# Kernel optimization log

Measured on AMD Instinct MI355X. Metric: run time of the kernel, lower is better.

## Reference

```python
import jax, jax.numpy as jnp
import numpy as np

EMBEDDING_DIM = 10
CONTEXT_SIZE_1 = 1
CONTEXT_SIZE_2 = 3
VOCAB = 50000
N = 1_000_000
NUM_NUMERIC = 16


def setup_inputs() -> dict:
    key = jax.random.key(0)
    ks = jax.random.split(key, 9)
    text_1 = jax.random.randint(ks[0], (N,), 0, VOCAB)
    text_2 = jax.random.randint(ks[1], (N,), 0, VOCAB)
    numeric_features = jax.random.normal(ks[2], (N, NUM_NUMERIC), dtype=jnp.float32)
    emb_table_1 = jax.random.normal(ks[3], (VOCAB, EMBEDDING_DIM), dtype=jnp.float32)
    emb_table_2 = jax.random.normal(ks[4], (VOCAB, EMBEDDING_DIM), dtype=jnp.float32)
    d_in = 2 * EMBEDDING_DIM + NUM_NUMERIC
    W1 = jax.random.normal(ks[5], (d_in, 128), dtype=jnp.float32) / np.sqrt(d_in)
    b1 = jnp.zeros((128,), dtype=jnp.float32)
    W2 = jax.random.normal(ks[6], (128, 1), dtype=jnp.float32) / np.sqrt(128.0)
    b2 = jnp.zeros((1,), dtype=jnp.float32)
    return {
        "text_1": text_1,
        "text_2": text_2,
        "numeric_features": numeric_features,
        "emb_table_1": emb_table_1,
        "emb_table_2": emb_table_2,
        "W1": W1,
        "b1": b1,
        "W2": W2,
        "b2": b2,
    }


def _contextual_embedding(ids, table, context_size):
    # mean of embeddings over window [i-cs, i+cs], clipped at sequence edges
    n = ids.shape[0]
    emb = table[ids]  # [N, D] gather
    # prefix sums with leading zero row: S[j] = sum(emb[0:j])
    S = jnp.concatenate([jnp.zeros((1, emb.shape[1]), emb.dtype),
                         jnp.cumsum(emb, axis=0)], axis=0)
    pos = jnp.arange(n)
    lo = jnp.maximum(pos - context_size, 0)
    hi = jnp.minimum(pos + context_size + 1, n)
    wsum = S[hi] - S[lo]                       # [N, D]
    count = (hi - lo).astype(emb.dtype)[:, None]
    return wsum / count


def reference(text_1, text_2, numeric_features, emb_table_1, emb_table_2, W1, b1, W2, b2):
    embed_1 = _contextual_embedding(text_1, emb_table_1, CONTEXT_SIZE_1)  # [N, 10]
    embed_2 = _contextual_embedding(text_2, emb_table_2, CONTEXT_SIZE_2)  # [N, 10]
    combined = jnp.concatenate([embed_1, embed_2, numeric_features], axis=1)
    h = jax.nn.relu(combined @ W1 + b1)
    out = h @ W2 + b2
    return jax.nn.sigmoid(out)  # [N, 1]
```

## Files before the change

### kernel.cpp

```cpp
#include <hip/hip_runtime.h>
#include <hip/hip_bf16.h>

#define EMB 10
#define DIN 36
#define HID 128
#define BM  128

typedef __attribute__((ext_vector_type(8))) short short8;
typedef __attribute__((ext_vector_type(4))) float f32x4;

__device__ __forceinline__ short bf16_hi(float v) {
  __hip_bfloat16 h = __float2bfloat16(v);
  return *reinterpret_cast<short*>(&h);
}
__device__ __forceinline__ float bf16_to_f(short s) {
  __hip_bfloat16 h = *reinterpret_cast<__hip_bfloat16*>(&s);
  return __bfloat162float(h);
}

__global__ void prep_kernel(const float* __restrict__ W1, const float* __restrict__ b1,
                            short* __restrict__ Bpack) {
  int b = blockIdx.x;
  int term = b >> 4;
  int ct   = (b >> 1) & 7;
  int ks   = b & 1;
  int l = threadIdx.x;
  int col = ct * 16 + (l & 15);
  int kb  = ks * 32 + (l >> 4) * 8;
  short8 o;
#pragma unroll
  for (int e = 0; e < 8; ++e) {
    int k = kb + e;
    float v = 0.0f;
    if (k < DIN)       v = W1[k * HID + col];
    else if (k == DIN) v = b1[col];
    short hb = bf16_hi(v);
    o[e] = (term == 0) ? hb : bf16_hi(v - bf16_to_f(hb));
  }
  *(short8*)(Bpack + (size_t)(((term * 8 + ct) * 2 + ks) * 64 + l) * 8) = o;
}

__global__ __launch_bounds__(256)
void fused_kernel(const int* __restrict__ t1, const int* __restrict__ t2,
                  const float* __restrict__ numf,
                  const float* __restrict__ tab1, const float* __restrict__ tab2,
                  const short* __restrict__ Bpack,
                  const float* __restrict__ W2, const float* __restrict__ b2,
                  float* __restrict__ out, int N) {
  __shared__ float E1[BM + 2][11];
  __shared__ float E2[BM + 6][11];
  __shared__ float Cs[BM][38];
  __shared__ float W2s[HID];

  const int tid = threadIdx.x;
  const long base = (long)blockIdx.x * BM;
  const int rloc = tid & 127;
  const int half = tid >> 7;
  const long rowm = base + rloc;

  float4 nfa, nfb;
  if (rowm < (long)N) {
    const float4* np = (const float4*)(numf + rowm * 16 + half * 8);
    nfa = np[0]; nfb = np[1];
  }

  if (tid < BM + 2) {
    long g = base - 1 + tid;
    if (g >= 0 && g < (long)N) {
      const float2* src = (const float2*)(tab1 + (long)t1[g] * EMB);
#pragma unroll
      for (int i = 0; i < 5; ++i) {
        float2 v = src[i];
        E1[tid][2 * i] = v.x; E1[tid][2 * i + 1] = v.y;
      }
    } else {
#pragma unroll
      for (int i = 0; i < EMB; ++i) E1[tid][i] = 0.0f;
    }
  }
  {
    int h = tid - (256 - (BM + 6));
    if (h >= 0) {
      long g = base - 3 + h;
      if (g >= 0 && g < (long)N) {
        const float2* src = (const float2*)(tab2 + (long)t2[g] * EMB);
#pragma unroll
        for (int i = 0; i < 5; ++i) {
          float2 v = src[i];
          E2[h][2 * i] = v.x; E2[h][2 * i + 1] = v.y;
        }
      } else {
#pragma unroll
        for (int i = 0; i < EMB; ++i) E2[h][i] = 0.0f;
      }
    }
  }
  if (tid < HID) W2s[tid] = W2[tid];
  __syncthreads();

  if (tid < 120) {
    int grp = tid / 10, d = tid - grp * 10;
    int r0 = grp * 11;
    float e[13];
#pragma unroll
    for (int i = 0; i < 13; ++i) {
      int h = r0 + i; if (h > 129) h = 129;
      e[i] = E1[h][d];
    }
#pragma unroll
    for (int i = 0; i < 11; ++i) {
      int rr = r0 + i;
      if (rr < BM) {
        long row = base + rr;
        float inv = 1.0f / 3.0f;
        if (row == 0 || row >= (long)N - 1) {
          long lo = row - 1; if (lo < 0) lo = 0;
          long hi = row + 2; if (hi > (long)N) hi = (long)N;
          long c = hi - lo;  if (c < 1) c = 1;
          inv = 1.0f / (float)c;
        }
        Cs[rr][d] = (e[i] + e[i + 1] + e[i + 2]) * inv;
      }
    }
  } else if (tid < 250) {
    int u = tid - 120;
    int grp = u / 10, d = u - grp * 10;
    int r0 = grp * 10;
    float e[16];
#pragma unroll
    for (int i = 0; i < 16; ++i) {
      int h = r0 + i; if (h > 133) h = 133;
      e[i] = E2[h][d];
    }
    float w = e[0] + e[1] + e[2] + e[3] + e[4] + e[5] + e[6];
#pragma unroll
    for (int i = 0; i < 10; ++i) {
      int rr = r0 + i;
      if (rr < BM) {
        long row = base + rr;
        float inv = 1.0f / 7.0f;
        if (row < 3 || row >= (long)N - 3) {
          long lo = row - 3; if (lo < 0) lo = 0;
          long hi = row + 4; if (hi > (long)N) hi = (long)N;
          long c = hi - lo;  if (c < 1) c = 1;
          inv = 1.0f / (float)c;
        }
        Cs[rr][10 + d] = w * inv;
      }
      if (i < 9) w += e[i + 7] - e[i];
    }
  }
  if (rowm < (long)N) {
    float* cp = &Cs[rloc][20 + half * 8];
    *(float2*)(cp + 0) = make_float2(nfa.x, nfa.y);
    *(float2*)(cp + 2) = make_float2(nfa.z, nfa.w);
    *(float2*)(cp + 4) = make_float2(nfb.x, nfb.y);
    *(float2*)(cp + 6) = make_float2(nfb.z, nfb.w);
    if (half == 0) *(float2*)(&Cs[rloc][36]) = make_float2(1.0f, 0.0f);
  }
  __syncthreads();

  const int wid = tid >> 6;
  const int l = tid & 63;
  const int arow = l & 15;
  const int kg = l >> 4;

  short8 aHi[2][2], aLo[2][2];
#pragma unroll
  for (int rtl = 0; rtl < 2; ++rtl) {
    const int r = (wid * 2 + rtl) * 16 + arow;
    const float* crow = &Cs[r][0];
    {
      float v[8];
#pragma unroll
      for (int i = 0; i < 4; ++i) {
        float2 t = *(const float2*)(crow + kg * 8 + 2 * i);
        v[2 * i] = t.x; v[2 * i + 1] = t.y;
      }
#pragma unroll
      for (int e = 0; e < 8; ++e) {
        short hb = bf16_hi(v[e]);
        aHi[rtl][0][e] = hb;
        aLo[rtl][0][e] = bf16_hi(v[e] - bf16_to_f(hb));
      }
    }
    if (kg == 0) {
      float v[8];
#pragma unroll
      for (int i = 0; i < 3; ++i) {
        float2 t = *(const float2*)(crow + 32 + 2 * i);
        v[2 * i] = t.x; v[2 * i + 1] = t.y;
      }
      v[6] = 0.0f; v[7] = 0.0f;
#pragma unroll
      for (int e = 0; e < 8; ++e) {
        short hb = bf16_hi(v[e]);
        aHi[rtl][1][e] = hb;
        aLo[rtl][1][e] = bf16_hi(v[e] - bf16_to_f(hb));
      }
    } else {
#pragma unroll
      for (int e = 0; e < 8; ++e) { aHi[rtl][1][e] = 0; aLo[rtl][1][e] = 0; }
    }
  }

  float part[2][4] = {{0,0,0,0},{0,0,0,0}};
#pragma unroll
  for (int ct = 0; ct < 8; ++ct) {
    short8 bb[2][2];
#pragma unroll
    for (int term = 0; term < 2; ++term)
#pragma unroll
      for (int ks = 0; ks < 2; ++ks)
        bb[term][ks] = *(const short8*)(Bpack +
            (size_t)(((term * 8 + ct) * 2 + ks) * 64 + l) * 8);
    float w2c = W2s[ct * 16 + (l & 15)];
#pragma unroll
    for (int rtl = 0; rtl < 2; ++rtl) {
      f32x4 acc = {0.0f, 0.0f, 0.0f, 0.0f};
#pragma unroll
      for (int ks = 0; ks < 2; ++ks) {
        acc = __builtin_amdgcn_mfma_f32_16x16x32_bf16(aHi[rtl][ks], bb[0][ks], acc, 0, 0, 0);
        acc = __builtin_amdgcn_mfma_f32_16x16x32_bf16(aLo[rtl][ks], bb[0][ks], acc, 0, 0, 0);
        acc = __builtin_amdgcn_mfma_f32_16x16x32_bf16(aHi[rtl][ks], bb[1][ks], acc, 0, 0, 0);
      }
#pragma unroll
      for (int r = 0; r < 4; ++r) {
        float hv = fmaxf(acc[r], 0.0f);
        part[rtl][r] += hv * w2c;
      }
    }
  }
#pragma unroll
  for (int off = 1; off < 16; off <<= 1) {
#pragma unroll
    for (int rtl = 0; rtl < 2; ++rtl)
#pragma unroll
      for (int r = 0; r < 4; ++r)
        part[rtl][r] += __shfl_xor(part[rtl][r], off, 64);
  }
  if ((l & 15) < 4) {
    float b2v = b2[0];
#pragma unroll
    for (int rtl = 0; rtl < 2; ++rtl) {
      int rt = wid * 2 + rtl;
      long grow = base + rt * 16 + (l >> 4) * 4 + (l & 15);
      if (grow < (long)N) {
        float x = part[rtl][l & 15] + b2v;
        out[grow] = 1.0f / (1.0f + expf(-x));
      }
    }
  }
}

extern "C" void kernel_launch(void* const* d_in, const int* in_sizes, int n_in,
                              void* d_out, int out_size, void* d_ws, size_t ws_size,
                              hipStream_t stream) {
  const int*   t1   = (const int*)d_in[0];
  const int*   t2   = (const int*)d_in[1];
  const float* numf = (const float*)d_in[2];
  const float* tab1 = (const float*)d_in[3];
  const float* tab2 = (const float*)d_in[4];
  const float* W1   = (const float*)d_in[5];
  const float* b1   = (const float*)d_in[6];
  const float* W2   = (const float*)d_in[7];
  const float* b2   = (const float*)d_in[8];
  float* out = (float*)d_out;
  const int N = in_sizes[0];
  short* Bpack = (short*)d_ws;

  hipLaunchKernelGGL(prep_kernel, dim3(32), dim3(64), 0, stream, W1, b1, Bpack);
  int nblk = (N + BM - 1) / BM;
  hipLaunchKernelGGL(fused_kernel, dim3(nblk), dim3(256), 0, stream,
                     t1, t2, numf, tab1, tab2, Bpack, W2, b2, out, N);
}
```

Before: 182.1 us.

## Load numeric features straight into MFMA registers, bypass LDS staging

Each lane now reads the numeric-feature columns it needs for its MFMA A fragments directly from global memory into registers, instead of staging them through the shared Cs tile, which shrinks from 38 to 22 columns. The hi/lo bf16 split is replaced with a truncation-based split using byte permutes. The window-sum edge handling moves to a block-level branch so interior blocks skip per-row boundary checks. The sigmoid uses exp2f. The trade-offs are less coalesced per-lane global loads and a truncating rather than rounding hi part, which the lo term should compensate for.

```diff
diff --git a/kernel.cpp b/kernel.cpp
--- a/kernel.cpp
+++ b/kernel.cpp
@@ -9,6 +9,8 @@
 typedef __attribute__((ext_vector_type(8))) short short8;
 typedef __attribute__((ext_vector_type(4))) float f32x4;
 
+union U8 { unsigned u[4]; short8 v; };
+
 __device__ __forceinline__ short bf16_hi(float v) {
   __hip_bfloat16 h = __float2bfloat16(v);
   return *reinterpret_cast<short*>(&h);
@@ -16,6 +18,14 @@
 __device__ __forceinline__ float bf16_to_f(short s) {
   __hip_bfloat16 h = *reinterpret_cast<__hip_bfloat16*>(&s);
   return __bfloat162float(h);
+}
+
+__device__ __forceinline__ void split_pair(float a, float b, unsigned &hi, unsigned &lo) {
+  unsigned ua = __float_as_uint(a), ub = __float_as_uint(b);
+  hi = __builtin_amdgcn_perm(ub, ua, 0x07060302u);
+  float ra = a - __uint_as_float(ua & 0xFFFF0000u);
+  float rb = b - __uint_as_float(ub & 0xFFFF0000u);
+  lo = __builtin_amdgcn_perm(__float_as_uint(rb), __float_as_uint(ra), 0x07060302u);
 }
 
 __global__ void prep_kernel(const float* __restrict__ W1, const float* __restrict__ b1,
@@ -47,24 +57,35 @@
                   const short* __restrict__ Bpack,
                   const float* __restrict__ W2, const float* __restrict__ b2,
                   float* __restrict__ out, int N) {
-  __shared__ float E1[BM + 2][11];
-  __shared__ float E2[BM + 6][11];
-  __shared__ float Cs[BM][38];
+  __shared__ float E1[134][11];
+  __shared__ float E2[136][11];
+  __shared__ float Cs[BM][22];
   __shared__ float W2s[HID];
 
   const int tid = threadIdx.x;
   const long base = (long)blockIdx.x * BM;
-  const int rloc = tid & 127;
-  const int half = tid >> 7;
-  const long rowm = base + rloc;
-
-  float4 nfa, nfb;
-  if (rowm < (long)N) {
-    const float4* np = (const float4*)(numf + rowm * 16 + half * 8);
-    nfa = np[0]; nfb = np[1];
-  }
-
-  if (tid < BM + 2) {
+  const int wid = tid >> 6;
+  const int l = tid & 63;
+  const int arow = l & 15;
+  const int kg = l >> 4;
+
+  const long rg0 = base + (long)(wid * 2) * 16 + arow;
+  const long rg1 = rg0 + 16;
+  float4 qa0 = {0,0,0,0}, qa1 = {0,0,0,0}, qb0 = {0,0,0,0}, qb1 = {0,0,0,0};
+  if (kg == 0) {
+    if (rg0 < (long)N) qa0 = *(const float4*)(numf + rg0 * 16 + 12);
+    if (rg1 < (long)N) qa1 = *(const float4*)(numf + rg1 * 16 + 12);
+  } else if (kg == 2) {
+    if (rg0 < (long)N) qa0 = *(const float4*)(numf + rg0 * 16);
+    if (rg1 < (long)N) qa1 = *(const float4*)(numf + rg1 * 16);
+  } else if (kg == 3) {
+    if (rg0 < (long)N) { qa0 = *(const float4*)(numf + rg0 * 16 + 4);
+                         qb0 = *(const float4*)(numf + rg0 * 16 + 8); }
+    if (rg1 < (long)N) { qa1 = *(const float4*)(numf + rg1 * 16 + 4);
+                         qb1 = *(const float4*)(numf + rg1 * 16 + 8); }
+  }
+
+  if (tid < 130) {
     long g = base - 1 + tid;
     if (g >= 0 && g < (long)N) {
       const float2* src = (const float2*)(tab1 + (long)t1[g] * EMB);
@@ -79,7 +100,7 @@
     }
   }
   {
-    int h = tid - (256 - (BM + 6));
+    int h = tid - 122;
     if (h >= 0) {
       long g = base - 3 + h;
       if (g >= 0 && g < (long)N) {
@@ -95,31 +116,33 @@
       }
     }
   }
-  if (tid < HID) W2s[tid] = W2[tid];
+  if (tid >= 128) W2s[tid - 128] = W2[tid - 128];
   __syncthreads();
 
+  const bool edgeblk = (base == 0) || (base + BM + 3 > (long)N);
   if (tid < 120) {
     int grp = tid / 10, d = tid - grp * 10;
     int r0 = grp * 11;
     float e[13];
 #pragma unroll
-    for (int i = 0; i < 13; ++i) {
-      int h = r0 + i; if (h > 129) h = 129;
-      e[i] = E1[h][d];
-    }
-#pragma unroll
-    for (int i = 0; i < 11; ++i) {
-      int rr = r0 + i;
-      if (rr < BM) {
-        long row = base + rr;
-        float inv = 1.0f / 3.0f;
-        if (row == 0 || row >= (long)N - 1) {
+    for (int i = 0; i < 13; ++i) e[i] = E1[r0 + i][d];
+    if (!edgeblk) {
+#pragma unroll
+      for (int i = 0; i < 11; ++i) {
+        int rr = r0 + i;
+        if (rr < BM) Cs[rr][d] = (e[i] + e[i + 1] + e[i + 2]) * (1.0f / 3.0f);
+      }
+    } else {
+#pragma unroll
+      for (int i = 0; i < 11; ++i) {
+        int rr = r0 + i;
+        if (rr < BM) {
+          long row = base + rr;
           long lo = row - 1; if (lo < 0) lo = 0;
           long hi = row + 2; if (hi > (long)N) hi = (long)N;
           long c = hi - lo;  if (c < 1) c = 1;
-          inv = 1.0f / (float)c;
+          Cs[rr][d] = (e[i] + e[i + 1] + e[i + 2]) / (float)c;
         }
-        Cs[rr][d] = (e[i] + e[i + 1] + e[i + 2]) * inv;
       }
     }
   } else if (tid < 250) {
@@ -128,80 +151,70 @@
     int r0 = grp * 10;
     float e[16];
 #pragma unroll
-    for (int i = 0; i < 16; ++i) {
-      int h = r0 + i; if (h > 133) h = 133;
-      e[i] = E2[h][d];
-    }
+    for (int i = 0; i < 16; ++i) e[i] = E2[r0 + i][d];
     float w = e[0] + e[1] + e[2] + e[3] + e[4] + e[5] + e[6];
-#pragma unroll
-    for (int i = 0; i < 10; ++i) {
-      int rr = r0 + i;
-      if (rr < BM) {
-        long row = base + rr;
-        float inv = 1.0f / 7.0f;
-        if (row < 3 || row >= (long)N - 3) {
+    if (!edgeblk) {
+#pragma unroll
+      for (int i = 0; i < 10; ++i) {
+        int rr = r0 + i;
+        if (rr < BM) Cs[rr][10 + d] = w * (1.0f / 7.0f);
+        if (i < 9) w += e[i + 7] - e[i];
+      }
+    } else {
+#pragma unroll
+      for (int i = 0; i < 10; ++i) {
+        int rr = r0 + i;
+        if (rr < BM) {
+          long row = base + rr;
           long lo = row - 3; if (lo < 0) lo = 0;
           long hi = row + 4; if (hi > (long)N) hi = (long)N;
           long c = hi - lo;  if (c < 1) c = 1;
-          inv = 1.0f / (float)c;
+          Cs[rr][10 + d] = w / (float)c;
         }
-        Cs[rr][10 + d] = w * inv;
-      }
-      if (i < 9) w += e[i + 7] - e[i];
-    }
-  }
-  if (rowm < (long)N) {
-    float* cp = &Cs[rloc][20 + half * 8];
-    *(float2*)(cp + 0) = make_float2(nfa.x, nfa.y);
-    *(float2*)(cp + 2) = make_float2(nfa.z, nfa.w);
-    *(float2*)(cp + 4) = make_float2(nfb.x, nfb.y);
-    *(float2*)(cp + 6) = make_float2(nfb.z, nfb.w);
-    if (half == 0) *(float2*)(&Cs[rloc][36]) = make_float2(1.0f, 0.0f);
+        if (i < 9) w += e[i + 7] - e[i];
+      }
+    }
   }
   __syncthreads();
-
-  const int wid = tid >> 6;
-  const int l = tid & 63;
-  const int arow = l & 15;
-  const int kg = l >> 4;
 
   short8 aHi[2][2], aLo[2][2];
 #pragma unroll
   for (int rtl = 0; rtl < 2; ++rtl) {
     const int r = (wid * 2 + rtl) * 16 + arow;
     const float* crow = &Cs[r][0];
-    {
-      float v[8];
+    const float4 qa = rtl ? qa1 : qa0;
+    const float4 qb = rtl ? qb1 : qb0;
+    U8 h0, l0, h1, l1;
+    if (kg <= 1) {
 #pragma unroll
       for (int i = 0; i < 4; ++i) {
         float2 t = *(const float2*)(crow + kg * 8 + 2 * i);
-        v[2 * i] = t.x; v[2 * i + 1] = t.y;
-      }
-#pragma unroll
-      for (int e = 0; e < 8; ++e) {
-        short hb = bf16_hi(v[e]);
-        aHi[rtl][0][e] = hb;
-        aLo[rtl][0][e] = bf16_hi(v[e] - bf16_to_f(hb));
-      }
+        split_pair(t.x, t.y, h0.u[i], l0.u[i]);
+      }
+    } else if (kg == 2) {
+      float2 t0 = *(const float2*)(crow + 16);
+      float2 t1 = *(const float2*)(crow + 18);
+      split_pair(t0.x, t0.y, h0.u[0], l0.u[0]);
+      split_pair(t1.x, t1.y, h0.u[1], l0.u[1]);
+      split_pair(qa.x, qa.y, h0.u[2], l0.u[2]);
+      split_pair(qa.z, qa.w, h0.u[3], l0.u[3]);
+    } else {
+      split_pair(qa.x, qa.y, h0.u[0], l0.u[0]);
+      split_pair(qa.z, qa.w, h0.u[1], l0.u[1]);
+      split_pair(qb.x, qb.y, h0.u[2], l0.u[2]);
+      split_pair(qb.z, qb.w, h0.u[3], l0.u[3]);
     }
     if (kg == 0) {
-      float v[8];
-#pragma unroll
-      for (int i = 0; i < 3; ++i) {
-        float2 t = *(const float2*)(crow + 32 + 2 * i);
-        v[2 * i] = t.x; v[2 * i + 1] = t.y;
-      }
-      v[6] = 0.0f; v[7] = 0.0f;
-#pragma unroll
-      for (int e = 0; e < 8; ++e) {
-        short hb = bf16_hi(v[e]);
-        aHi[rtl][1][e] = hb;
-        aLo[rtl][1][e] = bf16_hi(v[e] - bf16_to_f(hb));
-      }
-    } else {
-#pragma unroll
-      for (int e = 0; e < 8; ++e) { aHi[rtl][1][e] = 0; aLo[rtl][1][e] = 0; }
-    }
+      split_pair(qa.x, qa.y, h1.u[0], l1.u[0]);
+      split_pair(qa.z, qa.w, h1.u[1], l1.u[1]);
+      h1.u[2] = 0x00003F80u; l1.u[2] = 0u;
+      h1.u[3] = 0u;          l1.u[3] = 0u;
+    } else {
+      h1.u[0] = h1.u[1] = h1.u[2] = h1.u[3] = 0u;
+      l1.u[0] = l1.u[1] = l1.u[2] = l1.u[3] = 0u;
+    }
+    aHi[rtl][0] = h0.v; aLo[rtl][0] = l0.v;
+    aHi[rtl][1] = h1.v; aLo[rtl][1] = l1.v;
   }
 
   float part[2][4] = {{0,0,0,0},{0,0,0,0}};
@@ -247,7 +260,7 @@
       long grow = base + rt * 16 + (l >> 4) * 4 + (l & 15);
       if (grow < (long)N) {
         float x = part[rtl][l & 15] + b2v;
-        out[grow] = 1.0f / (1.0f + expf(-x));
+        out[grow] = 1.0f / (1.0f + exp2f(x * -1.44269504f));
       }
     }
   }
```

After: 183.3 us. No clear change (+0.6%).
